# Kernel tuning notes

Measured on AMD Instinct MI355X. Metric: run time of the kernel, lower is better.

Reference implementation:

```python
import jax, jax.numpy as jnp
import numpy as np

SOBEL_X = jnp.array([[1., 0., -1.], [2., 0., -2.], [1., 0., -1.]], dtype=jnp.float32)
SOBEL_Y = jnp.array([[1., 2., 1.], [0., 0., 0.], [-1., -2., -1.]], dtype=jnp.float32)


def _depthwise_sobel(x, k):
    # x: [B, C, H, W]; k: [3, 3]. Depthwise (per-channel) cross-correlation,
    # padding=1 (SAME), stride=1 -- matches torch Conv2d semantics (no flip).
    C = x.shape[1]
    kernel = jnp.broadcast_to(k, (C, 1, 3, 3))  # OIHW with groups=C
    return jax.lax.conv_general_dilated(
        x, kernel,
        window_strides=(1, 1),
        padding=((1, 1), (1, 1)),
        feature_group_count=C,
        dimension_numbers=('NCHW', 'OIHW', 'NCHW'))


def setup_inputs() -> dict:
    key = jax.random.key(0)
    k1, k2 = jax.random.split(key)
    B, C, H, W = 16, 64, 128, 128
    f1 = jax.random.normal(k1, (B, C, H, W), dtype=jnp.float32)
    f2 = jax.random.normal(k2, (B, C, H, W), dtype=jnp.float32)
    return {"f1": f1, "f2": f2}


def reference(f1, f2):
    sobel_x_f1 = _depthwise_sobel(f1, SOBEL_X)
    sobel_y_f1 = _depthwise_sobel(f1, SOBEL_Y)
    sobel_x_f2 = _depthwise_sobel(f2, SOBEL_X)
    sobel_y_f2 = _depthwise_sobel(f2, SOBEL_Y)
    return (sobel_x_f1, sobel_y_f1, sobel_x_f2, sobel_y_f2)
```

## Files before the change

### kernel.cpp

```cpp
#include <hip/hip_runtime.h>

#define BB 16
#define CC 64
#define HH 128
#define WW 128
#define TH 32
#define NTILES (HH / TH)
#define PLANES (BB*CC)
#define PLANE_SZ (HH*WW)
#define NTOT ((size_t)PLANES*PLANE_SZ)
#define LDW 132

typedef float f32x4 __attribute__((ext_vector_type(4)));

__global__ __launch_bounds__(256)
void sobel_fused_kernel(const float* __restrict__ f1,
                        const float* __restrict__ f2,
                        float* __restrict__ out) {
    __shared__ float tile[TH + 2][LDW];

    const int L  = blockIdx.x;
    const int s  = L >> 3;
    const int t  = s & 3;
    const int pg = ((s >> 2) << 3) + (L & 7);
    const int which = pg >> 10;
    const int plane = pg & 1023;

    const float* in = (which == 0 ? f1 : f2) + (size_t)plane * PLANE_SZ;
    float* out_sx = out + (size_t)(2 * which) * NTOT + (size_t)plane * PLANE_SZ;
    float* out_sy = out_sx + NTOT;

    const int y0  = t * TH;
    const int tid = threadIdx.x + threadIdx.y * 32;

    for (int idx = tid; idx < (TH + 2) * 32; idx += 256) {
        const int r  = idx >> 5;
        const int c4 = idx & 31;
        const int gy = y0 + r - 1;
        f32x4 v = {0.f, 0.f, 0.f, 0.f};
        if (gy >= 0 && gy < HH) {
            v = *reinterpret_cast<const f32x4*>(in + (size_t)gy * WW + c4 * 4);
        }
        float* dst = &tile[r][2 + c4 * 4];
        dst[0] = v.x; dst[1] = v.y; dst[2] = v.z; dst[3] = v.w;
    }
    if (tid < TH + 2) {
        tile[tid][0]   = 0.f;
        tile[tid][1]   = 0.f;
        tile[tid][130] = 0.f;
        tile[tid][131] = 0.f;
    }
    __syncthreads();

    const int tx = threadIdx.x;
    const int xb = tx * 4;

    #pragma unroll
    for (int rr = 0; rr < 4; ++rr) {
        const int ty = threadIdx.y + rr * 8;

        const f32x4 tA = *reinterpret_cast<const f32x4*>(&tile[ty][xb]);
        const f32x4 tB = *reinterpret_cast<const f32x4*>(&tile[ty][xb + 4]);
        const f32x4 mA = *reinterpret_cast<const f32x4*>(&tile[ty + 1][xb]);
        const f32x4 mB = *reinterpret_cast<const f32x4*>(&tile[ty + 1][xb + 4]);
        const f32x4 bA = *reinterpret_cast<const f32x4*>(&tile[ty + 2][xb]);
        const f32x4 bB = *reinterpret_cast<const f32x4*>(&tile[ty + 2][xb + 4]);

        const float t0 = tA.y, t1 = tA.z, t2 = tA.w, t3 = tB.x, t4 = tB.y, t5 = tB.z;
        const float m0 = mA.y, m1 = mA.z, m2 = mA.w, m3 = mB.x, m4 = mB.y, m5 = mB.z;
        const float b0 = bA.y, b1 = bA.z, b2 = bA.w, b3 = bB.x, b4 = bB.y, b5 = bB.z;

        f32x4 gx;
        gx.x = (t0 - t2) + 2.f * (m0 - m2) + (b0 - b2);
        gx.y = (t1 - t3) + 2.f * (m1 - m3) + (b1 - b3);
        gx.z = (t2 - t4) + 2.f * (m2 - m4) + (b2 - b4);
        gx.w = (t3 - t5) + 2.f * (m3 - m5) + (b3 - b5);

        f32x4 gy;
        gy.x = (t0 + 2.f * t1 + t2) - (b0 + 2.f * b1 + b2);
        gy.y = (t1 + 2.f * t2 + t3) - (b1 + 2.f * b2 + b3);
        gy.z = (t2 + 2.f * t3 + t4) - (b2 + 2.f * b3 + b4);
        gy.w = (t3 + 2.f * t4 + t5) - (b3 + 2.f * b4 + b5);

        const int orow = y0 + ty;
        __builtin_nontemporal_store(gx, reinterpret_cast<f32x4*>(out_sx + (size_t)orow * WW + xb));
        __builtin_nontemporal_store(gy, reinterpret_cast<f32x4*>(out_sy + (size_t)orow * WW + xb));
    }
}

extern "C" void kernel_launch(void* const* d_in, const int* in_sizes, int n_in,
                              void* d_out, int out_size, void* d_ws, size_t ws_size,
                              hipStream_t stream) {
    const float* f1 = (const float*)d_in[0];
    const float* f2 = (const float*)d_in[1];
    float* out = (float*)d_out;

    dim3 grid(NTILES * PLANES * 2);
    dim3 block(32, 8);
    sobel_fused_kernel<<<grid, block, 0, stream>>>(f1, f2, out);
}
```

Measured before the change: 369.2 us.

## Replace LDS tiling with per-thread register row streaming and lane shuffles

Drops the shared-memory tile and its barrier. Each thread now walks a 16-row band of one plane and keeps a sliding three-row window in registers. Horizontal neighbours come from wavefront shuffles, with the row edges zeroed by checking the lane. The grid shrinks to one block per plane, so each input row is loaded once per band, removing LDS traffic and synchronisation. The trade-off is fewer blocks, a longer serial chain per thread and more registers, which can limit how much memory latency is hidden.

```diff
diff --git a/kernel.cpp b/kernel.cpp
--- a/kernel.cpp
+++ b/kernel.cpp
@@ -1,90 +1,70 @@
 #include <hip/hip_runtime.h>
 
-#define BB 16
-#define CC 64
 #define HH 128
 #define WW 128
-#define TH 32
-#define NTILES (HH / TH)
-#define PLANES (BB*CC)
+#define PLANES 1024
 #define PLANE_SZ (HH*WW)
 #define NTOT ((size_t)PLANES*PLANE_SZ)
-#define LDW 132
+#define BAND 16
 
 typedef float f32x4 __attribute__((ext_vector_type(4)));
 
-__global__ __launch_bounds__(256)
+struct Win { float w0, w1, w2, w3, w4, w5; };
+
+__device__ __forceinline__ Win load_win(const float* __restrict__ in,
+                                        int y, int col, int tx) {
+    f32x4 v = {0.f, 0.f, 0.f, 0.f};
+    if (y >= 0 && y < HH)
+        v = *reinterpret_cast<const f32x4*>(in + y * WW + col);
+    const float lw = __shfl_up(v.w, 1);
+    const float rx = __shfl_down(v.x, 1);
+    Win w;
+    w.w0 = (tx == 0)  ? 0.f : lw;
+    w.w1 = v.x; w.w2 = v.y; w.w3 = v.z; w.w4 = v.w;
+    w.w5 = (tx == 31) ? 0.f : rx;
+    return w;
+}
+
+__global__ __launch_bounds__(256, 4)
 void sobel_fused_kernel(const float* __restrict__ f1,
                         const float* __restrict__ f2,
                         float* __restrict__ out) {
-    __shared__ float tile[TH + 2][LDW];
+    const int blk   = blockIdx.x;
+    const int which = blk >> 10;
+    const int plane = blk & 1023;
 
-    const int L  = blockIdx.x;
-    const int s  = L >> 3;
-    const int t  = s & 3;
-    const int pg = ((s >> 2) << 3) + (L & 7);
-    const int which = pg >> 10;
-    const int plane = pg & 1023;
-
-    const float* in = (which == 0 ? f1 : f2) + (size_t)plane * PLANE_SZ;
+    const float* in = (which ? f2 : f1) + (size_t)plane * PLANE_SZ;
     float* out_sx = out + (size_t)(2 * which) * NTOT + (size_t)plane * PLANE_SZ;
     float* out_sy = out_sx + NTOT;
 
-    const int y0  = t * TH;
-    const int tid = threadIdx.x + threadIdx.y * 32;
+    const int tx  = threadIdx.x;
+    const int col = tx * 4;
+    const int y0  = (int)threadIdx.y * BAND;
 
-    for (int idx = tid; idx < (TH + 2) * 32; idx += 256) {
-        const int r  = idx >> 5;
-        const int c4 = idx & 31;
-        const int gy = y0 + r - 1;
-        f32x4 v = {0.f, 0.f, 0.f, 0.f};
-        if (gy >= 0 && gy < HH) {
-            v = *reinterpret_cast<const f32x4*>(in + (size_t)gy * WW + c4 * 4);
-        }
-        float* dst = &tile[r][2 + c4 * 4];
-        dst[0] = v.x; dst[1] = v.y; dst[2] = v.z; dst[3] = v.w;
-    }
-    if (tid < TH + 2) {
-        tile[tid][0]   = 0.f;
-        tile[tid][1]   = 0.f;
-        tile[tid][130] = 0.f;
-        tile[tid][131] = 0.f;
-    }
-    __syncthreads();
-
-    const int tx = threadIdx.x;
-    const int xb = tx * 4;
+    Win rt = load_win(in, y0 - 1, col, tx);
+    Win rm = load_win(in, y0,     col, tx);
 
     #pragma unroll
-    for (int rr = 0; rr < 4; ++rr) {
-        const int ty = threadIdx.y + rr * 8;
-
-        const f32x4 tA = *reinterpret_cast<const f32x4*>(&tile[ty][xb]);
-        const f32x4 tB = *reinterpret_cast<const f32x4*>(&tile[ty][xb + 4]);
-        const f32x4 mA = *reinterpret_cast<const f32x4*>(&tile[ty + 1][xb]);
-        const f32x4 mB = *reinterpret_cast<const f32x4*>(&tile[ty + 1][xb + 4]);
-        const f32x4 bA = *reinterpret_cast<const f32x4*>(&tile[ty + 2][xb]);
-        const f32x4 bB = *reinterpret_cast<const f32x4*>(&tile[ty + 2][xb + 4]);
-
-        const float t0 = tA.y, t1 = tA.z, t2 = tA.w, t3 = tB.x, t4 = tB.y, t5 = tB.z;
-        const float m0 = mA.y, m1 = mA.z, m2 = mA.w, m3 = mB.x, m4 = mB.y, m5 = mB.z;
-        const float b0 = bA.y, b1 = bA.z, b2 = bA.w, b3 = bB.x, b4 = bB.y, b5 = bB.z;
+    for (int i = 0; i < BAND; ++i) {
+        const int y = y0 + i;
+        const Win rb = load_win(in, y + 1, col, tx);
 
         f32x4 gx;
-        gx.x = (t0 - t2) + 2.f * (m0 - m2) + (b0 - b2);
-        gx.y = (t1 - t3) + 2.f * (m1 - m3) + (b1 - b3);
-        gx.z = (t2 - t4) + 2.f * (m2 - m4) + (b2 - b4);
-        gx.w = (t3 - t5) + 2.f * (m3 - m5) + (b3 - b5);
+        gx.x = (rt.w0 - rt.w2) + 2.f * (rm.w0 - rm.w2) + (rb.w0 - rb.w2);
+        gx.y = (rt.w1 - rt.w3) + 2.f * (rm.w1 - rm.w3) + (rb.w1 - rb.w3);
+        gx.z = (rt.w2 - rt.w4) + 2.f * (rm.w2 - rm.w4) + (rb.w2 - rb.w4);
+        gx.w = (rt.w3 - rt.w5) + 2.f * (rm.w3 - rm.w5) + (rb.w3 - rb.w5);
 
         f32x4 gy;
-        gy.x = (t0 + 2.f * t1 + t2) - (b0 + 2.f * b1 + b2);
-        gy.y = (t1 + 2.f * t2 + t3) - (b1 + 2.f * b2 + b3);
-        gy.z = (t2 + 2.f * t3 + t4) - (b2 + 2.f * b3 + b4);
-        gy.w = (t3 + 2.f * t4 + t5) - (b3 + 2.f * b4 + b5);
+        gy.x = (rt.w0 + 2.f * rt.w1 + rt.w2) - (rb.w0 + 2.f * rb.w1 + rb.w2);
+        gy.y = (rt.w1 + 2.f * rt.w2 + rt.w3) - (rb.w1 + 2.f * rb.w2 + rb.w3);
+        gy.z = (rt.w2 + 2.f * rt.w3 + rt.w4) - (rb.w2 + 2.f * rb.w3 + rb.w4);
+        gy.w = (rt.w3 + 2.f * rt.w4 + rt.w5) - (rb.w3 + 2.f * rb.w4 + rb.w5);
 
-        const int orow = y0 + ty;
-        __builtin_nontemporal_store(gx, reinterpret_cast<f32x4*>(out_sx + (size_t)orow * WW + xb));
-        __builtin_nontemporal_store(gy, reinterpret_cast<f32x4*>(out_sy + (size_t)orow * WW + xb));
+        __builtin_nontemporal_store(gx, reinterpret_cast<f32x4*>(out_sx + (size_t)y * WW + col));
+        __builtin_nontemporal_store(gy, reinterpret_cast<f32x4*>(out_sy + (size_t)y * WW + col));
+
+        rt = rm; rm = rb;
     }
 }
 
@@ -95,7 +75,7 @@
     const float* f2 = (const float*)d_in[1];
     float* out = (float*)d_out;
 
-    dim3 grid(NTILES * PLANES * 2);
+    dim3 grid(PLANES * 2);
     dim3 block(32, 8);
     sobel_fused_kernel<<<grid, block, 0, stream>>>(f1, f2, out);
 }
```

New measurement: 366.2 us. About the same (-0.8%).
